# Performance work log

Hardware: AMD Instinct MI355X
Metric: run time of the kernel (lower is better)

The kernel has to match this reference:

```python
import jax, jax.numpy as jnp
import numpy as np

N = 1024      # n_nodes
S = 32        # state_dim
M = 32        # message_dim
STEPS = 5     # n_steps


def setup_inputs() -> dict:
    key = jax.random.key(0)
    ks = jax.random.split(key, 12)
    w = lambda k, shape: jax.random.normal(k, shape, jnp.float32) * 0.02
    return {
        "J": jax.random.normal(ks[0], (N, N), jnp.float32),
        "b": jax.random.normal(ks[1], (N,), jnp.float32),
        # message_passing MLP (Linear(2S+3->M), Linear(M->M), Linear(M->M))
        "W1": w(ks[2], (M, 2 * S + 3)), "b1": jnp.zeros((M,), jnp.float32),
        "W2": w(ks[3], (M, M)),         "b2": jnp.zeros((M,), jnp.float32),
        "W3": w(ks[4], (M, M)),         "b3": jnp.zeros((M,), jnp.float32),
        # GRU(input=S+M, hidden=S). h0 is always zero in the original forward,
        # so weight_hh never contributes (only bias_hh does) and is omitted.
        "W_ih": w(ks[5], (3 * S, S + M)),
        "b_ih": w(ks[6], (3 * S,)),
        "b_hh": w(ks[7], (3 * S,)),
        # readout MLP (Linear(S->M), Linear(M->M), Linear(M->2))
        "R1": w(ks[8], (M, S)),  "rb1": jnp.zeros((M,), jnp.float32),
        "R2": w(ks[9], (M, M)),  "rb2": jnp.zeros((M,), jnp.float32),
        "R3": w(ks[10], (2, M)), "rb3": jnp.zeros((2,), jnp.float32),
    }


def reference(J, b, W1, b1, W2, b2, W3, b3, W_ih, b_ih, b_hh, R1, rb1, R2, rb2, R3, rb3):
    # Split first linear over the concat [h_i, h_j, J_ij, b_i, b_j] so the
    # [N, N, 2S+3] concat tensor is never materialized.
    W1a, W1b = W1[:, :S], W1[:, S:2 * S]
    wJ, wbi, wbj = W1[:, 2 * S], W1[:, 2 * S + 1], W1[:, 2 * S + 2]

    def step(h, _):
        hi = h @ W1a.T                       # [N, M] (sender part)
        hj = h @ W1b.T                       # [N, M] (receiver part)
        pre = (hi[:, None, :] + hj[None, :, :]
               + J[:, :, None] * wJ
               + b[:, None, None] * wbi
               + b[None, :, None] * wbj
               + b1)                          # [N, N, M]
        x = jax.nn.relu(pre)
        x = jax.nn.relu(x @ W2.T + b2)
        x = jax.nn.relu(x @ W3.T + b3)       # message_i_j: [N, N, M]
        m = x.sum(0)                          # message to node j: sum over senders i
        # GRU with zero initial hidden state: h' = (1-z) * n_gate
        gi = jnp.concatenate([h, m], axis=-1) @ W_ih.T + b_ih  # [N, 3S]
        r = jax.nn.sigmoid(gi[:, :S] + b_hh[:S])
        z = jax.nn.sigmoid(gi[:, S:2 * S] + b_hh[S:2 * S])
        n = jnp.tanh(gi[:, 2 * S:] + r * b_hh[2 * S:])
        return (1.0 - z) * n, None

    h0 = jnp.zeros((N, S), J.dtype)
    h, _ = jax.lax.scan(step, h0, None, length=STEPS)

    r = jax.nn.relu(h @ R1.T + rb1)
    r = jax.nn.relu(r @ R2.T + rb2)
    r = jax.nn.relu(r @ R3.T + rb3)          # [N, 2]
    return jax.nn.sigmoid(r)
```

## Files before the change

### kernel.cpp

```cpp
#include <hip/hip_runtime.h>
#include <math.h>

#define NN 1024

typedef __attribute__((ext_vector_type(8))) short bf16x8;
typedef __attribute__((ext_vector_type(4))) float f32x4;
typedef __attribute__((ext_vector_type(4))) unsigned int u32x4;

__device__ __forceinline__ float sigmoidf_(float x) { return 1.0f / (1.0f + __expf(-x)); }

__device__ __forceinline__ unsigned int pk2(float a, float b) {
    return __builtin_amdgcn_perm(__float_as_uint(a) + 0x8000u,
                                 __float_as_uint(b) + 0x8000u, 0x03020706u);
}
__device__ __forceinline__ unsigned short f2bf_rne(float a) {
    unsigned int ua = __float_as_uint(a);
    ua += 0x7fffu + ((ua >> 16) & 1u);
    return (unsigned short)(ua >> 16);
}

#define CFG_FLOATS 2560

__global__ __launch_bounds__(256) void k_pre(
    const float* __restrict__ J, const float* __restrict__ b,
    const float* __restrict__ W1, const float* __restrict__ b1,
    const float* __restrict__ W2, const float* __restrict__ b2,
    const float* __restrict__ W3, const float* __restrict__ b3,
    float* __restrict__ Jt, float* __restrict__ h,
    float* __restrict__ u0, float* __restrict__ v, float* __restrict__ cfg)
{
    __shared__ float tile[32][33];
    const int t = blockIdx.x;
    const int tid = threadIdx.x;
    if (t < 1024) {
        int tx = (t & 31) * 32, ty = (t >> 5) * 32;
        int x = tid & 31, y = tid >> 5;
#pragma unroll
        for (int r = 0; r < 4; r++)
            tile[y + 8 * r][x] = J[(size_t)(ty + y + 8 * r) * NN + tx + x];
        __syncthreads();
#pragma unroll
        for (int r = 0; r < 4; r++)
            Jt[(size_t)(tx + y + 8 * r) * NN + ty + x] = tile[x][y + 8 * r];
    } else if (t < 1152) {
        int idx = (t - 1024) * 256 + tid;
        int row = idx >> 5, mm = idx & 31;
        float bi = b[row];
        h[idx]  = 0.f;
        u0[idx] = bi * W1[mm * 67 + 65];
        v[idx]  = fmaf(bi, W1[mm * 67 + 66], b1[mm]);
    } else if (tid < 64) {
        const int l = tid, p = l & 15, q = l >> 4;
        union FU { unsigned int d[4]; unsigned short s[8]; } t0, t1, t2, t3;
        float wj[8];
#pragma unroll
        for (int jj = 0; jj < 8; jj++) {
            int k = q * 8 + jj;
            t0.s[jj] = f2bf_rne(W2[p * 32 + k]);
            t1.s[jj] = f2bf_rne(W2[(16 + p) * 32 + k]);
            t2.s[jj] = f2bf_rne(W3[p * 32 + k]);
            t3.s[jj] = f2bf_rne(W3[(16 + p) * 32 + k]);
            wj[jj] = W1[k * 67 + 64];
        }
        u32x4* cw = (u32x4*)cfg;
        cw[l]       = *(u32x4*)t0.d;
        cw[64 + l]  = *(u32x4*)t1.d;
        cw[128 + l] = *(u32x4*)t2.d;
        cw[192 + l] = *(u32x4*)t3.d;
        f32x4* cf = (f32x4*)(cfg + 1024);
        f32x4 v0, v1, v2, v3;
#pragma unroll
        for (int r = 0; r < 4; r++) {
            v0[r] = b2[q * 4 + r];  v1[r] = b2[16 + q * 4 + r];
            v2[r] = b3[q * 4 + r];  v3[r] = b3[16 + q * 4 + r];
        }
        cf[l] = v0; cf[64 + l] = v1; cf[128 + l] = v2; cf[192 + l] = v3;
        f32x4* cj = (f32x4*)(cfg + 2048);
        f32x4 wlo, whi;
#pragma unroll
        for (int r = 0; r < 4; r++) { wlo[r] = wj[r]; whi[r] = wj[4 + r]; }
        cj[l] = wlo; cj[64 + l] = whi;
    }
}

__global__ __launch_bounds__(256, 4) void k_step(
    const float* __restrict__ Jt, const float* __restrict__ cfg,
    const float* __restrict__ Wih, const float* __restrict__ bih,
    const float* __restrict__ bhh, const float* __restrict__ b,
    const float* __restrict__ b1, const float* __restrict__ W1,
    const float* __restrict__ R1, const float* __restrict__ rb1,
    const float* __restrict__ R2, const float* __restrict__ rb2,
    const float* __restrict__ R3, const float* __restrict__ rb3,
    float* __restrict__ h, float* __restrict__ v,
    const float* __restrict__ ui, float* __restrict__ uo,
    float* __restrict__ out, int do_out)
{
    __shared__ float red[4 * 32];
    __shared__ float hm[64], gbuf[96], hnb[32], tb[32];

    const int tid = threadIdx.x;
    const int w = tid >> 6;
    const int l = tid & 63;
    const int p = l & 15;
    const int q = l >> 4;
    const int j = blockIdx.x;

    union FU { bf16x8 v; u32x4 u4; } w2a0, w2a1, w3a0, w3a1;
    const u32x4* cw = (const u32x4*)cfg;
    w2a0.u4 = cw[l]; w2a1.u4 = cw[64 + l]; w3a0.u4 = cw[128 + l]; w3a1.u4 = cw[192 + l];
    const f32x4* cf = (const f32x4*)(cfg + 1024);
    const f32x4 b2v0 = cf[l], b2v1 = cf[64 + l], b3v0 = cf[128 + l], b3v1 = cf[192 + l];
    const f32x4* cj = (const f32x4*)(cfg + 2048);
    const f32x4 wlo = cj[l], whi = cj[64 + l];
    float wj8[8];
#pragma unroll
    for (int r = 0; r < 4; r++) { wj8[r] = wlo[r]; wj8[4 + r] = whi[r]; }

    float vv[8];
    {
        float4 va = *(const float4*)(v + j * 32 + q * 8);
        float4 vb = *(const float4*)(v + j * 32 + q * 8 + 4);
        vv[0] = va.x; vv[1] = va.y; vv[2] = va.z; vv[3] = va.w;
        vv[4] = vb.x; vv[5] = vb.y; vv[6] = vb.z; vv[7] = vb.w;
    }

    const float* Jtrow = Jt + (size_t)j * NN;
    const int s0 = (p | ((l & 16) << 1)) << 2;
    const int s1 = s0 + 64;
    const bool qlo = (l & 32) == 0;

    f32x4 acc0 = {0.f, 0.f, 0.f, 0.f}, acc1 = {0.f, 0.f, 0.f, 0.f};

    const int ibase = w * 256;
    float  jwA = Jtrow[ibase + p];
    float4 uaA = *(const float4*)(ui + (ibase + p) * 32 + q * 8);
    float4 ubA = *(const float4*)(ui + (ibase + p) * 32 + q * 8 + 4);
    float  jwB = Jtrow[ibase + 16 + p];
    float4 uaB = *(const float4*)(ui + (ibase + 16 + p) * 32 + q * 8);
    float4 ubB = *(const float4*)(ui + (ibase + 16 + p) * 32 + q * 8 + 4);

#pragma unroll 4
    for (int t = 0; t < 16; ++t) {
        float  jw_c;
        float4 ua_c, ub_c;
        if ((t & 1) == 0) { jw_c = jwA; ua_c = uaA; ub_c = ubA; }
        else              { jw_c = jwB; ua_c = uaB; ub_c = ubB; }
        if (t < 14) {
            const int in = ibase + (t + 2) * 16 + p;
            if ((t & 1) == 0) {
                jwA = Jtrow[in];
                uaA = *(const float4*)(ui + in * 32 + q * 8);
                ubA = *(const float4*)(ui + in * 32 + q * 8 + 4);
            } else {
                jwB = Jtrow[in];
                uaB = *(const float4*)(ui + in * 32 + q * 8);
                ubB = *(const float4*)(ui + in * 32 + q * 8 + 4);
            }
        }

        float xr[8];
        xr[0] = fmaxf(fmaf(jw_c, wj8[0], ua_c.x + vv[0]), 0.f);
        xr[1] = fmaxf(fmaf(jw_c, wj8[1], ua_c.y + vv[1]), 0.f);
        xr[2] = fmaxf(fmaf(jw_c, wj8[2], ua_c.z + vv[2]), 0.f);
        xr[3] = fmaxf(fmaf(jw_c, wj8[3], ua_c.w + vv[3]), 0.f);
        xr[4] = fmaxf(fmaf(jw_c, wj8[4], ub_c.x + vv[4]), 0.f);
        xr[5] = fmaxf(fmaf(jw_c, wj8[5], ub_c.y + vv[5]), 0.f);
        xr[6] = fmaxf(fmaf(jw_c, wj8[6], ub_c.z + vv[6]), 0.f);
        xr[7] = fmaxf(fmaf(jw_c, wj8[7], ub_c.w + vv[7]), 0.f);

        union BU { u32x4 u4; bf16x8 v; unsigned int d[4]; } bx;
        bx.d[0] = pk2(xr[0], xr[1]);
        bx.d[1] = pk2(xr[2], xr[3]);
        bx.d[2] = pk2(xr[4], xr[5]);
        bx.d[3] = pk2(xr[6], xr[7]);

        f32x4 c0 = __builtin_amdgcn_mfma_f32_16x16x32_bf16(w2a0.v, bx.v, b2v0, 0, 0, 0);
        f32x4 c1 = __builtin_amdgcn_mfma_f32_16x16x32_bf16(w2a1.v, bx.v, b2v1, 0, 0, 0);

        const int d0 = (int)pk2(fmaxf(c0[0], 0.f), fmaxf(c0[1], 0.f));
        const int d1 = (int)pk2(fmaxf(c0[2], 0.f), fmaxf(c0[3], 0.f));
        const int d2 = (int)pk2(fmaxf(c1[0], 0.f), fmaxf(c1[1], 0.f));
        const int d3 = (int)pk2(fmaxf(c1[2], 0.f), fmaxf(c1[3], 0.f));

        const int A0 = __builtin_amdgcn_ds_bpermute(s0, d0);
        const int A1 = __builtin_amdgcn_ds_bpermute(s0, d1);
        const int A2 = __builtin_amdgcn_ds_bpermute(s1, d0);
        const int A3 = __builtin_amdgcn_ds_bpermute(s1, d1);
        const int B0 = __builtin_amdgcn_ds_bpermute(s0, d2);
        const int B1 = __builtin_amdgcn_ds_bpermute(s0, d3);
        const int B2 = __builtin_amdgcn_ds_bpermute(s1, d2);
        const int B3 = __builtin_amdgcn_ds_bpermute(s1, d3);

        union BU yr;
        yr.d[0] = (unsigned)(qlo ? A0 : B0);
        yr.d[1] = (unsigned)(qlo ? A1 : B1);
        yr.d[2] = (unsigned)(qlo ? A2 : B2);
        yr.d[3] = (unsigned)(qlo ? A3 : B3);

        f32x4 e0 = __builtin_amdgcn_mfma_f32_16x16x32_bf16(w3a0.v, yr.v, b3v0, 0, 0, 0);
        f32x4 e1 = __builtin_amdgcn_mfma_f32_16x16x32_bf16(w3a1.v, yr.v, b3v1, 0, 0, 0);
#pragma unroll
        for (int r = 0; r < 4; r++) {
            acc0[r] += fmaxf(e0[r], 0.f);
            acc1[r] += fmaxf(e1[r], 0.f);
        }
    }

#pragma unroll
    for (int bit = 1; bit < 16; bit <<= 1) {
#pragma unroll
        for (int r = 0; r < 4; r++) {
            acc0[r] += __shfl_xor(acc0[r], bit);
            acc1[r] += __shfl_xor(acc1[r], bit);
        }
    }
    if (p == 0) {
#pragma unroll
        for (int r = 0; r < 4; r++) {
            red[w * 32 + q * 4 + r]      = acc0[r];
            red[w * 32 + 16 + q * 4 + r] = acc1[r];
        }
    }
    __syncthreads();

    if (tid < 64) {
        float val;
        if (tid < 32) val = h[j * 32 + tid];
        else {
            int s = tid - 32;
            val = red[s] + red[32 + s] + red[64 + s] + red[96 + s];
        }
        hm[tid] = val;
    }
    __syncthreads();

    if (tid < 192) {
        const int row = tid >> 1, half = tid & 1;
        const float* wr = Wih + row * 64 + half * 32;
        const float* hh = hm + half * 32;
        float acc = 0.f;
#pragma unroll
        for (int k4 = 0; k4 < 8; k4++) {
            float4 w4 = *(const float4*)(wr + 4 * k4);
            acc = fmaf(w4.x, hh[4 * k4 + 0], acc);
            acc = fmaf(w4.y, hh[4 * k4 + 1], acc);
            acc = fmaf(w4.z, hh[4 * k4 + 2], acc);
            acc = fmaf(w4.w, hh[4 * k4 + 3], acc);
        }
        acc += __shfl_xor(acc, 1);
        if (half == 0) gbuf[row] = acc + bih[row];
    }
    __syncthreads();

    if (tid < 32) {
        const int s = tid;
        float r = sigmoidf_(gbuf[s] + bhh[s]);
        float z = sigmoidf_(gbuf[32 + s] + bhh[32 + s]);
        float n = tanhf(gbuf[64 + s] + r * bhh[64 + s]);
        float hn_ = (1.0f - z) * n;
        hnb[s] = hn_;
        h[j * 32 + s] = hn_;
    }
    __syncthreads();

    if (tid < 64) {
        const int s = tid & 31;
        const bool isV = tid >= 32;
        const float bj = b[j];
        const float* wr = W1 + s * 67 + (isV ? 32 : 0);
        float acc = isV ? fmaf(bj, W1[s * 67 + 66], b1[s]) : bj * W1[s * 67 + 65];
#pragma unroll
        for (int k = 0; k < 32; k++) acc = fmaf(wr[k], hnb[k], acc);
        if (isV) v[j * 32 + s] = acc;
        else     uo[j * 32 + s] = acc;
    }

    if (do_out) {
        __syncthreads();
        if (tid < 32) {
            float a = rb1[tid];
            const float* rr = R1 + tid * 32;
#pragma unroll 8
            for (int k = 0; k < 32; k++) a = fmaf(rr[k], hnb[k], a);
            gbuf[tid] = fmaxf(a, 0.f);
        }
        __syncthreads();
        if (tid < 32) {
            float a = rb2[tid];
            const float* rr = R2 + tid * 32;
#pragma unroll 8
            for (int k = 0; k < 32; k++) a = fmaf(rr[k], gbuf[k], a);
            tb[tid] = fmaxf(a, 0.f);
        }
        __syncthreads();
        if (tid < 2) {
            float a = rb3[tid];
            const float* rr = R3 + tid * 32;
#pragma unroll 8
            for (int k = 0; k < 32; k++) a = fmaf(rr[k], tb[k], a);
            out[j * 2 + tid] = sigmoidf_(fmaxf(a, 0.f));
        }
    }
}

extern "C" void kernel_launch(void* const* d_in, const int* in_sizes, int n_in,
                              void* d_out, int out_size, void* d_ws, size_t ws_size,
                              hipStream_t stream)
{
    const float* J   = (const float*)d_in[0];
    const float* b   = (const float*)d_in[1];
    const float* W1  = (const float*)d_in[2];
    const float* b1  = (const float*)d_in[3];
    const float* W2  = (const float*)d_in[4];
    const float* b2  = (const float*)d_in[5];
    const float* W3  = (const float*)d_in[6];
    const float* b3  = (const float*)d_in[7];
    const float* Wih = (const float*)d_in[8];
    const float* bih = (const float*)d_in[9];
    const float* bhh = (const float*)d_in[10];
    const float* R1  = (const float*)d_in[11];
    const float* rb1 = (const float*)d_in[12];
    const float* R2  = (const float*)d_in[13];
    const float* rb2 = (const float*)d_in[14];
    const float* R3  = (const float*)d_in[15];
    const float* rb3 = (const float*)d_in[16];

    float* out = (float*)d_out;
    float* ws  = (float*)d_ws;
    float* h   = ws;
    float* v   = ws + 32768;
    float* u0  = ws + 65536;
    float* u1  = ws + 98304;
    float* Jt  = ws + 131072;
    float* cfg = ws + 131072 + NN * NN;

    k_pre<<<1153, 256, 0, stream>>>(J, b, W1, b1, W2, b2, W3, b3,
                                    Jt, h, u0, v, cfg);
    for (int s = 0; s < 5; s++) {
        const float* ui = (s & 1) ? u1 : u0;
        float*       uo = (s & 1) ? u0 : u1;
        k_step<<<1024, 256, 0, stream>>>(Jt, cfg, Wih, bih, bhh, b, b1, W1,
                                         R1, rb1, R2, rb2, R3, rb3,
                                         h, v, ui, uo, out, (s == 4) ? 1 : 0);
    }
}
```

Measured before the change: 200.9 us.

## Split step kernel into message and GRU kernels, halve sender range per block

The fused step kernel is split into k_main, which computes message partial sums over half the senders per block using 2048 blocks, and k_tail, which adds the two partials and runs the GRU update. The intent is to raise parallelism and shorten per-block serial work, and to keep the cheap GRU tail from holding the MFMA-heavy kernel's registers. The elementwise math is also vectorised with float2/float4 max ops, and a hardware packed bf16 convert is used where the compiler supports it. This adds an extra launch and a global round trip for the partials in each step, and the packed convert may round differently from the old add-and-truncate packing.

```diff
diff --git a/kernel.cpp b/kernel.cpp
--- a/kernel.cpp
+++ b/kernel.cpp
@@ -5,6 +5,7 @@
 
 typedef __attribute__((ext_vector_type(8))) short bf16x8;
 typedef __attribute__((ext_vector_type(4))) float f32x4;
+typedef __attribute__((ext_vector_type(2))) float f32x2;
 typedef __attribute__((ext_vector_type(4))) unsigned int u32x4;
 
 __device__ __forceinline__ float sigmoidf_(float x) { return 1.0f / (1.0f + __expf(-x)); }
@@ -12,6 +13,13 @@
 __device__ __forceinline__ unsigned int pk2(float a, float b) {
     return __builtin_amdgcn_perm(__float_as_uint(a) + 0x8000u,
                                  __float_as_uint(b) + 0x8000u, 0x03020706u);
+}
+__device__ __forceinline__ unsigned int pkcvt(float a, float b) {
+#if __has_builtin(__builtin_amdgcn_cvt_pk_bf16_f32)
+    return __builtin_bit_cast(unsigned int, __builtin_amdgcn_cvt_pk_bf16_f32(a, b));
+#else
+    return pk2(a, b);
+#endif
 }
 __device__ __forceinline__ unsigned short f2bf_rne(float a) {
     unsigned int ua = __float_as_uint(a);
@@ -83,8 +91,156 @@
     }
 }
 
-__global__ __launch_bounds__(256, 4) void k_step(
+__device__ __forceinline__ void tile_body(
+    float jw, const float4& ua_c, const float4& ub_c,
+    const f32x2* vv2, const f32x2* wj2,
+    const bf16x8& w2a0, const bf16x8& w2a1,
+    const bf16x8& w3a0, const bf16x8& w3a1,
+    const f32x4& b2v0, const f32x4& b2v1,
+    const f32x4& b3v0, const f32x4& b3v1,
+    int s0, int s1, bool qlo, f32x4& acc0, f32x4& acc1)
+{
+    const f32x2 jw2 = {jw, jw};
+    const f32x2 z2 = {0.f, 0.f};
+    const f32x4 z4 = {0.f, 0.f, 0.f, 0.f};
+
+    f32x2 x0 = {ua_c.x, ua_c.y}, x1 = {ua_c.z, ua_c.w};
+    f32x2 x2 = {ub_c.x, ub_c.y}, x3 = {ub_c.z, ub_c.w};
+    x0 = jw2 * wj2[0] + (x0 + vv2[0]);
+    x1 = jw2 * wj2[1] + (x1 + vv2[1]);
+    x2 = jw2 * wj2[2] + (x2 + vv2[2]);
+    x3 = jw2 * wj2[3] + (x3 + vv2[3]);
+    x0 = __builtin_elementwise_max(x0, z2);
+    x1 = __builtin_elementwise_max(x1, z2);
+    x2 = __builtin_elementwise_max(x2, z2);
+    x3 = __builtin_elementwise_max(x3, z2);
+
+    union BU { u32x4 u4; bf16x8 v; unsigned int d[4]; } bx;
+    bx.d[0] = pkcvt(x0[0], x0[1]);
+    bx.d[1] = pkcvt(x1[0], x1[1]);
+    bx.d[2] = pkcvt(x2[0], x2[1]);
+    bx.d[3] = pkcvt(x3[0], x3[1]);
+
+    f32x4 c0 = __builtin_amdgcn_mfma_f32_16x16x32_bf16(w2a0, bx.v, b2v0, 0, 0, 0);
+    f32x4 c1 = __builtin_amdgcn_mfma_f32_16x16x32_bf16(w2a1, bx.v, b2v1, 0, 0, 0);
+    c0 = __builtin_elementwise_max(c0, z4);
+    c1 = __builtin_elementwise_max(c1, z4);
+
+    const int d0 = (int)pkcvt(c0[0], c0[1]);
+    const int d1 = (int)pkcvt(c0[2], c0[3]);
+    const int d2 = (int)pkcvt(c1[0], c1[1]);
+    const int d3 = (int)pkcvt(c1[2], c1[3]);
+
+    const int A0 = __builtin_amdgcn_ds_bpermute(s0, d0);
+    const int A1 = __builtin_amdgcn_ds_bpermute(s0, d1);
+    const int A2 = __builtin_amdgcn_ds_bpermute(s1, d0);
+    const int A3 = __builtin_amdgcn_ds_bpermute(s1, d1);
+    const int B0 = __builtin_amdgcn_ds_bpermute(s0, d2);
+    const int B1 = __builtin_amdgcn_ds_bpermute(s0, d3);
+    const int B2 = __builtin_amdgcn_ds_bpermute(s1, d2);
+    const int B3 = __builtin_amdgcn_ds_bpermute(s1, d3);
+
+    union BU yr;
+    yr.d[0] = (unsigned)(qlo ? A0 : B0);
+    yr.d[1] = (unsigned)(qlo ? A1 : B1);
+    yr.d[2] = (unsigned)(qlo ? A2 : B2);
+    yr.d[3] = (unsigned)(qlo ? A3 : B3);
+
+    f32x4 e0 = __builtin_amdgcn_mfma_f32_16x16x32_bf16(w3a0, yr.v, b3v0, 0, 0, 0);
+    f32x4 e1 = __builtin_amdgcn_mfma_f32_16x16x32_bf16(w3a1, yr.v, b3v1, 0, 0, 0);
+    acc0 = acc0 + __builtin_elementwise_max(e0, z4);
+    acc1 = acc1 + __builtin_elementwise_max(e1, z4);
+}
+
+__global__ __launch_bounds__(256, 4) void k_main(
     const float* __restrict__ Jt, const float* __restrict__ cfg,
+    const float* __restrict__ v, const float* __restrict__ ui,
+    float* __restrict__ mpart)
+{
+    __shared__ float red[4 * 32];
+    const int tid = threadIdx.x;
+    const int w = tid >> 6;
+    const int l = tid & 63;
+    const int p = l & 15;
+    const int q = l >> 4;
+    const int j = blockIdx.x >> 1;
+    const int half = blockIdx.x & 1;
+
+    union FU { bf16x8 v; u32x4 u4; } w2a0, w2a1, w3a0, w3a1;
+    const u32x4* cw = (const u32x4*)cfg;
+    w2a0.u4 = cw[l]; w2a1.u4 = cw[64 + l]; w3a0.u4 = cw[128 + l]; w3a1.u4 = cw[192 + l];
+    const f32x4* cf = (const f32x4*)(cfg + 1024);
+    const f32x4 b2v0 = cf[l], b2v1 = cf[64 + l], b3v0 = cf[128 + l], b3v1 = cf[192 + l];
+    const f32x4* cj = (const f32x4*)(cfg + 2048);
+    const f32x4 wlo = cj[l], whi = cj[64 + l];
+    f32x2 wj2[4] = { {wlo[0], wlo[1]}, {wlo[2], wlo[3]}, {whi[0], whi[1]}, {whi[2], whi[3]} };
+
+    f32x2 vv2[4];
+    {
+        float4 va = *(const float4*)(v + j * 32 + q * 8);
+        float4 vb = *(const float4*)(v + j * 32 + q * 8 + 4);
+        vv2[0] = f32x2{va.x, va.y}; vv2[1] = f32x2{va.z, va.w};
+        vv2[2] = f32x2{vb.x, vb.y}; vv2[3] = f32x2{vb.z, vb.w};
+    }
+
+    const float* Jtrow = Jt + (size_t)j * NN;
+    const int s0 = (p | ((l & 16) << 1)) << 2;
+    const int s1 = s0 + 64;
+    const bool qlo = (l & 32) == 0;
+
+    f32x4 acc0 = {0.f, 0.f, 0.f, 0.f}, acc1 = {0.f, 0.f, 0.f, 0.f};
+
+    const int ibase = half * 512 + w * 128;
+    int iA = ibase + p, iB = ibase + 16 + p;
+    float  jwA = Jtrow[iA];
+    float4 uaA = *(const float4*)(ui + iA * 32 + q * 8);
+    float4 ubA = *(const float4*)(ui + iA * 32 + q * 8 + 4);
+    float  jwB = Jtrow[iB];
+    float4 uaB = *(const float4*)(ui + iB * 32 + q * 8);
+    float4 ubB = *(const float4*)(ui + iB * 32 + q * 8 + 4);
+
+#pragma unroll
+    for (int tt = 0; tt < 4; ++tt) {
+        const float  jwA_c = jwA; const float4 uaA_c = uaA, ubA_c = ubA;
+        const float  jwB_c = jwB; const float4 uaB_c = uaB, ubB_c = ubB;
+        if (tt < 3) {
+            const int inA = ibase + (2 * tt + 2) * 16 + p;
+            const int inB = inA + 16;
+            jwA = Jtrow[inA];
+            uaA = *(const float4*)(ui + inA * 32 + q * 8);
+            ubA = *(const float4*)(ui + inA * 32 + q * 8 + 4);
+            jwB = Jtrow[inB];
+            uaB = *(const float4*)(ui + inB * 32 + q * 8);
+            ubB = *(const float4*)(ui + inB * 32 + q * 8 + 4);
+        }
+        tile_body(jwA_c, uaA_c, ubA_c, vv2, wj2, w2a0.v, w2a1.v, w3a0.v, w3a1.v,
+                  b2v0, b2v1, b3v0, b3v1, s0, s1, qlo, acc0, acc1);
+        tile_body(jwB_c, uaB_c, ubB_c, vv2, wj2, w2a0.v, w2a1.v, w3a0.v, w3a1.v,
+                  b2v0, b2v1, b3v0, b3v1, s0, s1, qlo, acc0, acc1);
+    }
+
+#pragma unroll
+    for (int bit = 1; bit < 16; bit <<= 1) {
+#pragma unroll
+        for (int r = 0; r < 4; r++) {
+            acc0[r] += __shfl_xor(acc0[r], bit);
+            acc1[r] += __shfl_xor(acc1[r], bit);
+        }
+    }
+    if (p == 0) {
+#pragma unroll
+        for (int r = 0; r < 4; r++) {
+            red[w * 32 + q * 4 + r]      = acc0[r];
+            red[w * 32 + 16 + q * 4 + r] = acc1[r];
+        }
+    }
+    __syncthreads();
+    if (tid < 32)
+        mpart[(half << 15) + j * 32 + tid] =
+            red[tid] + red[32 + tid] + red[64 + tid] + red[96 + tid];
+}
+
+__global__ __launch_bounds__(256) void k_tail(
     const float* __restrict__ Wih, const float* __restrict__ bih,
     const float* __restrict__ bhh, const float* __restrict__ b,
     const float* __restrict__ b1, const float* __restrict__ W1,
@@ -92,143 +248,19 @@
     const float* __restrict__ R2, const float* __restrict__ rb2,
     const float* __restrict__ R3, const float* __restrict__ rb3,
     float* __restrict__ h, float* __restrict__ v,
-    const float* __restrict__ ui, float* __restrict__ uo,
+    const float* __restrict__ mpart, float* __restrict__ uo,
     float* __restrict__ out, int do_out)
 {
-    __shared__ float red[4 * 32];
     __shared__ float hm[64], gbuf[96], hnb[32], tb[32];
-
     const int tid = threadIdx.x;
-    const int w = tid >> 6;
-    const int l = tid & 63;
-    const int p = l & 15;
-    const int q = l >> 4;
     const int j = blockIdx.x;
-
-    union FU { bf16x8 v; u32x4 u4; } w2a0, w2a1, w3a0, w3a1;
-    const u32x4* cw = (const u32x4*)cfg;
-    w2a0.u4 = cw[l]; w2a1.u4 = cw[64 + l]; w3a0.u4 = cw[128 + l]; w3a1.u4 = cw[192 + l];
-    const f32x4* cf = (const f32x4*)(cfg + 1024);
-    const f32x4 b2v0 = cf[l], b2v1 = cf[64 + l], b3v0 = cf[128 + l], b3v1 = cf[192 + l];
-    const f32x4* cj = (const f32x4*)(cfg + 2048);
-    const f32x4 wlo = cj[l], whi = cj[64 + l];
-    float wj8[8];
-#pragma unroll
-    for (int r = 0; r < 4; r++) { wj8[r] = wlo[r]; wj8[4 + r] = whi[r]; }
-
-    float vv[8];
-    {
-        float4 va = *(const float4*)(v + j * 32 + q * 8);
-        float4 vb = *(const float4*)(v + j * 32 + q * 8 + 4);
-        vv[0] = va.x; vv[1] = va.y; vv[2] = va.z; vv[3] = va.w;
-        vv[4] = vb.x; vv[5] = vb.y; vv[6] = vb.z; vv[7] = vb.w;
-    }
-
-    const float* Jtrow = Jt + (size_t)j * NN;
-    const int s0 = (p | ((l & 16) << 1)) << 2;
-    const int s1 = s0 + 64;
-    const bool qlo = (l & 32) == 0;
-
-    f32x4 acc0 = {0.f, 0.f, 0.f, 0.f}, acc1 = {0.f, 0.f, 0.f, 0.f};
-
-    const int ibase = w * 256;
-    float  jwA = Jtrow[ibase + p];
-    float4 uaA = *(const float4*)(ui + (ibase + p) * 32 + q * 8);
-    float4 ubA = *(const float4*)(ui + (ibase + p) * 32 + q * 8 + 4);
-    float  jwB = Jtrow[ibase + 16 + p];
-    float4 uaB = *(const float4*)(ui + (ibase + 16 + p) * 32 + q * 8);
-    float4 ubB = *(const float4*)(ui + (ibase + 16 + p) * 32 + q * 8 + 4);
-
-#pragma unroll 4
-    for (int t = 0; t < 16; ++t) {
-        float  jw_c;
-        float4 ua_c, ub_c;
-        if ((t & 1) == 0) { jw_c = jwA; ua_c = uaA; ub_c = ubA; }
-        else              { jw_c = jwB; ua_c = uaB; ub_c = ubB; }
-        if (t < 14) {
-            const int in = ibase + (t + 2) * 16 + p;
-            if ((t & 1) == 0) {
-                jwA = Jtrow[in];
-                uaA = *(const float4*)(ui + in * 32 + q * 8);
-                ubA = *(const float4*)(ui + in * 32 + q * 8 + 4);
-            } else {
-                jwB = Jtrow[in];
-                uaB = *(const float4*)(ui + in * 32 + q * 8);
-                ubB = *(const float4*)(ui + in * 32 + q * 8 + 4);
-            }
-        }
-
-        float xr[8];
-        xr[0] = fmaxf(fmaf(jw_c, wj8[0], ua_c.x + vv[0]), 0.f);
-        xr[1] = fmaxf(fmaf(jw_c, wj8[1], ua_c.y + vv[1]), 0.f);
-        xr[2] = fmaxf(fmaf(jw_c, wj8[2], ua_c.z + vv[2]), 0.f);
-        xr[3] = fmaxf(fmaf(jw_c, wj8[3], ua_c.w + vv[3]), 0.f);
-        xr[4] = fmaxf(fmaf(jw_c, wj8[4], ub_c.x + vv[4]), 0.f);
-        xr[5] = fmaxf(fmaf(jw_c, wj8[5], ub_c.y + vv[5]), 0.f);
-        xr[6] = fmaxf(fmaf(jw_c, wj8[6], ub_c.z + vv[6]), 0.f);
-        xr[7] = fmaxf(fmaf(jw_c, wj8[7], ub_c.w + vv[7]), 0.f);
-
-        union BU { u32x4 u4; bf16x8 v; unsigned int d[4]; } bx;
-        bx.d[0] = pk2(xr[0], xr[1]);
-        bx.d[1] = pk2(xr[2], xr[3]);
-        bx.d[2] = pk2(xr[4], xr[5]);
-        bx.d[3] = pk2(xr[6], xr[7]);
-
-        f32x4 c0 = __builtin_amdgcn_mfma_f32_16x16x32_bf16(w2a0.v, bx.v, b2v0, 0, 0, 0);
-        f32x4 c1 = __builtin_amdgcn_mfma_f32_16x16x32_bf16(w2a1.v, bx.v, b2v1, 0, 0, 0);
-
-        const int d0 = (int)pk2(fmaxf(c0[0], 0.f), fmaxf(c0[1], 0.f));
-        const int d1 = (int)pk2(fmaxf(c0[2], 0.f), fmaxf(c0[3], 0.f));
-        const int d2 = (int)pk2(fmaxf(c1[0], 0.f), fmaxf(c1[1], 0.f));
-        const int d3 = (int)pk2(fmaxf(c1[2], 0.f), fmaxf(c1[3], 0.f));
-
-        const int A0 = __builtin_amdgcn_ds_bpermute(s0, d0);
-        const int A1 = __builtin_amdgcn_ds_bpermute(s0, d1);
-        const int A2 = __builtin_amdgcn_ds_bpermute(s1, d0);
-        const int A3 = __builtin_amdgcn_ds_bpermute(s1, d1);
-        const int B0 = __builtin_amdgcn_ds_bpermute(s0, d2);
-        const int B1 = __builtin_amdgcn_ds_bpermute(s0, d3);
-        const int B2 = __builtin_amdgcn_ds_bpermute(s1, d2);
-        const int B3 = __builtin_amdgcn_ds_bpermute(s1, d3);
-
-        union BU yr;
-        yr.d[0] = (unsigned)(qlo ? A0 : B0);
-        yr.d[1] = (unsigned)(qlo ? A1 : B1);
-        yr.d[2] = (unsigned)(qlo ? A2 : B2);
-        yr.d[3] = (unsigned)(qlo ? A3 : B3);
-
-        f32x4 e0 = __builtin_amdgcn_mfma_f32_16x16x32_bf16(w3a0.v, yr.v, b3v0, 0, 0, 0);
-        f32x4 e1 = __builtin_amdgcn_mfma_f32_16x16x32_bf16(w3a1.v, yr.v, b3v1, 0, 0, 0);
-#pragma unroll
-        for (int r = 0; r < 4; r++) {
-            acc0[r] += fmaxf(e0[r], 0.f);
-            acc1[r] += fmaxf(e1[r], 0.f);
-        }
-    }
-
-#pragma unroll
-    for (int bit = 1; bit < 16; bit <<= 1) {
-#pragma unroll
-        for (int r = 0; r < 4; r++) {
-            acc0[r] += __shfl_xor(acc0[r], bit);
-            acc1[r] += __shfl_xor(acc1[r], bit);
-        }
-    }
-    if (p == 0) {
-#pragma unroll
-        for (int r = 0; r < 4; r++) {
-            red[w * 32 + q * 4 + r]      = acc0[r];
-            red[w * 32 + 16 + q * 4 + r] = acc1[r];
-        }
-    }
-    __syncthreads();
 
     if (tid < 64) {
         float val;
         if (tid < 32) val = h[j * 32 + tid];
         else {
             int s = tid - 32;
-            val = red[s] + red[32 + s] + red[64 + s] + red[96 + s];
+            val = mpart[j * 32 + s] + mpart[32768 + j * 32 + s];
         }
         hm[tid] = val;
     }
@@ -327,20 +359,22 @@
 
     float* out = (float*)d_out;
     float* ws  = (float*)d_ws;
-    float* h   = ws;
-    float* v   = ws + 32768;
-    float* u0  = ws + 65536;
-    float* u1  = ws + 98304;
-    float* Jt  = ws + 131072;
-    float* cfg = ws + 131072 + NN * NN;
+    float* h     = ws;
+    float* v     = ws + 32768;
+    float* u0    = ws + 65536;
+    float* u1    = ws + 98304;
+    float* Jt    = ws + 131072;
+    float* cfg   = ws + 131072 + NN * NN;
+    float* mpart = cfg + CFG_FLOATS;
 
     k_pre<<<1153, 256, 0, stream>>>(J, b, W1, b1, W2, b2, W3, b3,
                                     Jt, h, u0, v, cfg);
     for (int s = 0; s < 5; s++) {
         const float* ui = (s & 1) ? u1 : u0;
         float*       uo = (s & 1) ? u0 : u1;
-        k_step<<<1024, 256, 0, stream>>>(Jt, cfg, Wih, bih, bhh, b, b1, W1,
+        k_main<<<2048, 256, 0, stream>>>(Jt, cfg, v, ui, mpart);
+        k_tail<<<1024, 256, 0, stream>>>(Wih, bih, bhh, b, b1, W1,
                                          R1, rb1, R2, rb2, R3, rb3,
-                                         h, v, ui, uo, out, (s == 4) ? 1 : 0);
-    }
-}
+                                         h, v, mpart, uo, out, (s == 4) ? 1 : 0);
+    }
+}
```

Measured after the change: 229.4 us. +14.2%, slower.
